# Optimization experiments

Hardware: AMD Instinct MI355X
Metric: run time of the kernel (lower is better)

Reference implementation:

```python
import jax, jax.numpy as jnp
import numpy as np

B, C, F, T = 4, 64, 64, 128
IC = 32  # inter_channels = C // 2
EPS = 1e-5  # BatchNorm eps


def _conv1x1(x, w, b=None):
    # x: (B, Cin, H, W), w: (Cout, Cin)
    y = jnp.einsum('bchw,oc->bohw', x, w)
    if b is not None:
        y = y + b[None, :, None, None]
    return y


def _maxpool2(x):
    b, c, h, w = x.shape
    return x.reshape(b, c, h // 2, 2, w // 2, 2).max(axis=(3, 5))


def _pos_score(fsz, tsz, h2_w):
    # positional encoding is (fpos, tpos) in [0,1]; the 2->1 conv head makes the
    # pos_delta contribution separable: score(n,m) = s(n) - s(m)
    fpos = jnp.linspace(0.0, 1.0, fsz)
    tpos = jnp.linspace(0.0, 1.0, tsz)
    return (h2_w[0] * fpos[:, None] + h2_w[1] * tpos[None, :]).reshape(-1)


def setup_inputs() -> dict:
    key = jax.random.key(0)
    ks = jax.random.split(key, 16)
    s = 0.05
    inp = {
        'x': jax.random.normal(ks[0], (B, C, F, T), dtype=jnp.float32),
        'psi_w': jax.random.normal(ks[1], (IC, C)) * s,
        'psi_b': jax.random.normal(ks[2], (IC,)) * s,
        'theta_w': jax.random.normal(ks[3], (IC, C)) * s,
        'theta_b': jax.random.normal(ks[4], (IC,)) * s,
        'phi_w': jax.random.normal(ks[5], (IC, C)) * s,
        'phi_b': jax.random.normal(ks[6], (IC,)) * s,
        'h0_w': jax.random.normal(ks[7], (IC,)) * s,
        'h1_w': jax.random.normal(ks[8], (IC,)) * s,
        'h2_w': jax.random.normal(ks[9], (2,)) * s,
        'W_w': jax.random.normal(ks[10], (C, IC + 1)) * s,
        'W_b': jax.random.normal(ks[11], (C,)) * s,
        'bn_gamma': jax.random.normal(ks[12], (C,)) * s + 1.0,
        'bn_beta': jax.random.normal(ks[13], (C,)) * s,
        'bn_mean': jax.random.normal(ks[14], (C,)) * s,
        'bn_var': jax.random.uniform(ks[15], (C,), minval=0.5, maxval=1.5),
    }
    return inp


def reference(x, psi_w, psi_b, theta_w, theta_b, phi_w, phi_b,
              h0_w, h1_w, h2_w, W_w, W_b, bn_gamma, bn_beta, bn_mean, bn_var):
    Bs, Cs, Fs, Ts = x.shape
    N = Fs * Ts
    M = (Fs // 2) * (Ts // 2)

    psi_x = _maxpool2(_conv1x1(x, psi_w, psi_b))      # (B, IC, F/2, T/2)
    theta_x = _conv1x1(x, theta_w, theta_b)           # (B, IC, F, T)
    phi_x = _maxpool2(_conv1x1(x, phi_w, phi_b))      # (B, IC, F/2, T/2)

    # additive attention scores: relu(head0(theta) + head1(phi) + head2(pos_delta))
    t_score = jnp.einsum('bcft,c->bft', theta_x, h0_w).reshape(Bs, N)   # (B, N)
    p_score = jnp.einsum('bcft,c->bft', phi_x, h1_w).reshape(Bs, M)     # (B, M)
    a = _pos_score(Fs, Ts, h2_w)             # (N,) query pos contribution
    bpos = _pos_score(Fs // 2, Ts // 2, h2_w)  # (M,) key pos contribution
    f = jax.nn.relu((t_score + a[None, :])[:, :, None]
                    + (p_score - bpos[None, :])[:, None, :])  # (B, N, M)

    f_div = f / jnp.asarray(M, f.dtype)
    psi_flat = psi_x.reshape(Bs, IC, M)
    y = jnp.einsum('bnm,bcm->bcn', f_div, psi_flat).reshape(Bs, IC, Fs, Ts)

    # r_structure_type='zero' -> structure feature is zeros (1 extra channel)
    structure = jnp.zeros((Bs, 1, Fs, Ts), dtype=y.dtype)
    y = jnp.concatenate([y, structure], axis=1)       # (B, IC+1, F, T)

    wy = _conv1x1(y, W_w, W_b)                        # (B, C, F, T)
    inv = bn_gamma / jnp.sqrt(bn_var + EPS)
    wy = wy * inv[None, :, None, None] + (bn_beta - bn_mean * inv)[None, :, None, None]
    return wy + x
```

## Files before the change

kernel.cpp:

```cpp
#include <hip/hip_runtime.h>

#define B_ 4
#define C_ 64
#define F_ 64
#define T_ 128
#define IC_ 32
#define N_ 8192
#define M_ 2048

#define OFF_U      0
#define OFF_PSI2   32768
#define OFF_V      294912
#define OFF_VS     303104
#define OFF_Q0     311296
#define OFF_Q1     835840
#define WS_FLOATS  1360384

__device__ __align__(16) float g_ws[WS_FLOATS];
__device__ int g_perm[B_ * M_];

__global__ __launch_bounds__(256) void k_front(
    const float* __restrict__ x,
    const float* __restrict__ psi_w, const float* __restrict__ psi_b,
    const float* __restrict__ theta_w, const float* __restrict__ theta_b,
    const float* __restrict__ phi_w, const float* __restrict__ phi_b,
    const float* __restrict__ h0_w, const float* __restrict__ h1_w,
    const float* __restrict__ h2_w)
{
    float* __restrict__ ws = g_ws;
    __shared__ __align__(16) float xs[64 * 64];
    __shared__ float pw[32 * 65];
    __shared__ float fw[32 * 65];
    __shared__ float wt_l[64];

    const int tid = threadIdx.x;
    const int bid = blockIdx.x;
    const int b = bid >> 7;
    const int rem = bid & 127;
    const int fh = rem >> 2;
    const int q = rem & 3;
    const int c0 = q * 32;

    for (int idx = tid; idx < 4096; idx += 256) {
        int c = idx >> 6, r2 = (idx >> 5) & 1, tl = idx & 31;
        xs[idx] = x[(((size_t)b * 64 + c) * 64 + (2 * fh + r2)) * 128 + c0 + tl];
    }
    for (int idx = tid; idx < 2048; idx += 256) {
        int o = idx >> 6, c = idx & 63;
        pw[o * 65 + c] = psi_w[idx];
        fw[o * 65 + c] = phi_w[idx];
    }
    if (tid < 64) {
        float acc = 0.f;
        for (int o2 = 0; o2 < 32; ++o2)
            acc += h0_w[o2] * theta_w[o2 * 64 + tid];
        wt_l[tid] = acc;
    }
    __syncthreads();

    const float h20 = h2_w[0], h21 = h2_w[1];

    {
        const int o = tid & 31, g = tid >> 5;
        const float pb = psi_b[o], fb = phi_b[o], h1 = h1_w[o];
        float sp[2][4] = {{0,0,0,0},{0,0,0,0}};
        float sf[2][4] = {{0,0,0,0},{0,0,0,0}};
        const int hc0 = g, hc1 = g + 8;
        for (int c = 0; c < 64; ++c) {
            const float pwv = pw[o * 65 + c];
            const float fwv = fw[o * 65 + c];
            const float2 xa0 = *(const float2*)&xs[c * 64 + 2 * hc0];
            const float2 xb0 = *(const float2*)&xs[c * 64 + 32 + 2 * hc0];
            const float2 xa1 = *(const float2*)&xs[c * 64 + 2 * hc1];
            const float2 xb1 = *(const float2*)&xs[c * 64 + 32 + 2 * hc1];
            sp[0][0] += pwv * xa0.x; sp[0][1] += pwv * xa0.y;
            sp[0][2] += pwv * xb0.x; sp[0][3] += pwv * xb0.y;
            sf[0][0] += fwv * xa0.x; sf[0][1] += fwv * xa0.y;
            sf[0][2] += fwv * xb0.x; sf[0][3] += fwv * xb0.y;
            sp[1][0] += pwv * xa1.x; sp[1][1] += pwv * xa1.y;
            sp[1][2] += pwv * xb1.x; sp[1][3] += pwv * xb1.y;
            sf[1][0] += fwv * xa1.x; sf[1][1] += fwv * xa1.y;
            sf[1][2] += fwv * xb1.x; sf[1][3] += fwv * xb1.y;
        }
#pragma unroll
        for (int h = 0; h < 2; ++h) {
            const int hc = h ? hc1 : hc0;
            const float psiv = fmaxf(fmaxf(sp[h][0], sp[h][1]), fmaxf(sp[h][2], sp[h][3])) + pb;
            const float phiv = fmaxf(fmaxf(sf[h][0], sf[h][1]), fmaxf(sf[h][2], sf[h][3])) + fb;
            const int m = fh * 64 + q * 16 + hc;
            ws[OFF_PSI2 + ((size_t)b * 2048 + m) * 32 + o] = psiv;
            float tv = h1 * phiv;
            for (int mask = 1; mask < 32; mask <<= 1)
                tv += __shfl_xor(tv, mask, 64);
            if (o == 0) {
                const float bpos = h20 * (fh * (1.0f / 31.0f))
                                 + h21 * ((q * 16 + hc) * (1.0f / 63.0f));
                ws[OFF_V + b * 2048 + m] = tv - bpos;
            }
        }
    }

    if (tid < 64) {
        const int r2 = tid >> 5, tl = tid & 31;
        float acc = 0.f;
        for (int c = 0; c < 64; ++c)
            acc += xs[c * 64 + r2 * 32 + tl] * wt_l[c];
        float tb_ = 0.f;
        for (int o2 = 0; o2 < 32; ++o2)
            tb_ += h0_w[o2] * theta_b[o2];
        const int f = 2 * fh + r2, tt = c0 + tl;
        const int n = f * 128 + tt;
        const float a = h20 * (f * (1.0f / 63.0f)) + h21 * (tt * (1.0f / 127.0f));
        ws[OFF_U + b * 8192 + n] = acc + tb_ + a;
    }
}

__global__ __launch_bounds__(256) void k_rank()
{
    float* __restrict__ ws = g_ws;
    __shared__ __align__(16) float vl[2048];
    __shared__ int part[256];
    const int tid = threadIdx.x;
    const int b = blockIdx.x >> 7, chunk = blockIdx.x & 127;
    const float* v = ws + OFF_V + b * 2048;
    for (int i = tid; i < 2048; i += 256) vl[i] = v[i];
    __syncthreads();

    const int ml = tid & 15, jq = tid >> 4;
    const int m = chunk * 16 + ml;
    const float vm = vl[m];
    int cnt = 0;
    const float4* v4 = (const float4*)vl;
    const int j0 = jq * 32;
    for (int j4 = j0; j4 < j0 + 32; ++j4) {
        const float4 vv = v4[j4];
        const int jb = j4 * 4;
        cnt += (vv.x > vm) || (vv.x == vm && (jb    ) < m);
        cnt += (vv.y > vm) || (vv.y == vm && (jb + 1) < m);
        cnt += (vv.z > vm) || (vv.z == vm && (jb + 2) < m);
        cnt += (vv.w > vm) || (vv.w == vm && (jb + 3) < m);
    }
    part[tid] = cnt;
    __syncthreads();
    if (tid < 16) {
        int r = 0;
#pragma unroll
        for (int j = 0; j < 16; ++j) r += part[j * 16 + tid];
        ws[OFF_VS + b * 2048 + r] = vl[chunk * 16 + tid];
        g_perm[b * 2048 + r] = chunk * 16 + tid;
    }
}

__global__ __launch_bounds__(512) void k_scan(
    const float* __restrict__ W_w)
{
    float* __restrict__ ws = g_ws;
    __shared__ float Wrow[32];
    __shared__ float a0[512], a1[512];
    const int tid = threadIdx.x;
    const int b = blockIdx.x >> 6, o = blockIdx.x & 63;
    if (tid < 32) Wrow[tid] = W_w[o * 33 + tid];
    __syncthreads();

    const int* perm = g_perm + b * 2048;
    const float* vs = ws + OFF_VS + b * 2048;
    const float* psi2 = ws + OFF_PSI2 + (size_t)b * 2048 * 32;

    float zl[4], vlv[4];
    float s0 = 0.f, s1 = 0.f;
    const int base = tid * 4;
#pragma unroll
    for (int qq = 0; qq < 4; ++qq) {
        const int i = base + qq;
        const int mp = perm[i];
        const float4* pr = (const float4*)(psi2 + (size_t)mp * 32);
        float z = 0.f;
#pragma unroll
        for (int w = 0; w < 8; ++w) {
            const float4 p4 = pr[w];
            z += Wrow[4 * w] * p4.x + Wrow[4 * w + 1] * p4.y
               + Wrow[4 * w + 2] * p4.z + Wrow[4 * w + 3] * p4.w;
        }
        const float vv = vs[i];
        zl[qq] = z; vlv[qq] = vv;
        s0 += z; s1 += vv * z;
    }
    a0[tid] = s0; a1[tid] = s1;
    __syncthreads();
    for (int off = 1; off < 512; off <<= 1) {
        const float t0_ = (tid >= off) ? a0[tid - off] : 0.f;
        const float t1_ = (tid >= off) ? a1[tid - off] : 0.f;
        __syncthreads();
        a0[tid] += t0_; a1[tid] += t1_;
        __syncthreads();
    }
    float r0 = a0[tid] - s0, r1 = a1[tid] - s1;
    float* Q0 = ws + OFF_Q0 + (size_t)b * 2049 * 64;
    float* Q1 = ws + OFF_Q1 + (size_t)b * 2049 * 64;
#pragma unroll
    for (int qq = 0; qq < 4; ++qq) {
        r0 += zl[qq]; r1 += vlv[qq] * zl[qq];
        Q0[(size_t)(base + qq + 1) * 64 + o] = r0;
        Q1[(size_t)(base + qq + 1) * 64 + o] = r1;
    }
    if (tid == 0) { Q0[o] = 0.f; Q1[o] = 0.f; }
}

__global__ __launch_bounds__(512) void k_out(
    const float* __restrict__ x,
    const float* __restrict__ W_b,
    const float* __restrict__ bn_g, const float* __restrict__ bn_b,
    const float* __restrict__ bn_m, const float* __restrict__ bn_v,
    float* __restrict__ out)
{
    const float* __restrict__ ws = g_ws;
    __shared__ float tileb[64 * 65];
    __shared__ int karr[64];
    __shared__ float uarr[64];

    const int tid = threadIdx.x;
    const int b = blockIdx.x >> 7, tile = blockIdx.x & 127;
    const int n0 = tile * 64;

    const float* vs = ws + OFF_VS + b * 2048;
    if (tid < 64) {
        const float u = ws[OFF_U + b * 8192 + n0 + tid];
        const float thr = -u;
        int lo = 0, hi = 2048;
        while (lo < hi) {
            const int mid = (lo + hi) >> 1;
            if (vs[mid] > thr) lo = mid + 1; else hi = mid;
        }
        karr[tid] = lo;
        uarr[tid] = u;
    }
    __syncthreads();

    const int lane = tid & 63, w = tid >> 6;
    const float inv = bn_g[lane] * __frsqrt_rn(bn_v[lane] + 1e-5f);
    const float sft = W_b[lane] * inv + bn_b[lane] - bn_m[lane] * inv;
    const float* Q0 = ws + OFF_Q0 + (size_t)b * 2049 * 64;
    const float* Q1 = ws + OFF_Q1 + (size_t)b * 2049 * 64;

    for (int nl = w; nl < 64; nl += 8) {
        const int k = karr[nl];
        const float u = uarr[nl];
        const float q0 = Q0[(size_t)k * 64 + lane];
        const float q1 = Q1[(size_t)k * 64 + lane];
        const float raw = (u * q0 + q1) * (1.0f / 2048.0f);
        tileb[lane * 65 + nl] = raw * inv + sft;
    }
    __syncthreads();

    for (int idx = tid; idx < 2048; idx += 512) {
        const int o = idx >> 5, j2 = idx & 31;
        const size_t gi = ((size_t)b * 64 + o) * 8192 + n0 + 2 * j2;
        const float2 xv = *(const float2*)&x[gi];
        float2 r;
        r.x = tileb[o * 65 + 2 * j2] + xv.x;
        r.y = tileb[o * 65 + 2 * j2 + 1] + xv.y;
        *(float2*)&out[gi] = r;
    }
}

extern "C" void kernel_launch(void* const* d_in, const int* in_sizes, int n_in,
                              void* d_out, int out_size, void* d_ws, size_t ws_size,
                              hipStream_t stream)
{
    (void)in_sizes; (void)n_in; (void)out_size; (void)d_ws; (void)ws_size;
    const float* x       = (const float*)d_in[0];
    const float* psi_w   = (const float*)d_in[1];
    const float* psi_b   = (const float*)d_in[2];
    const float* theta_w = (const float*)d_in[3];
    const float* theta_b = (const float*)d_in[4];
    const float* phi_w   = (const float*)d_in[5];
    const float* phi_b   = (const float*)d_in[6];
    const float* h0_w    = (const float*)d_in[7];
    const float* h1_w    = (const float*)d_in[8];
    const float* h2_w    = (const float*)d_in[9];
    const float* W_w     = (const float*)d_in[10];
    const float* W_b     = (const float*)d_in[11];
    const float* bn_g    = (const float*)d_in[12];
    const float* bn_b    = (const float*)d_in[13];
    const float* bn_m    = (const float*)d_in[14];
    const float* bn_v    = (const float*)d_in[15];
    float* out = (float*)d_out;

    k_front<<<dim3(512), dim3(256), 0, stream>>>(x, psi_w, psi_b, theta_w, theta_b,
                                                 phi_w, phi_b, h0_w, h1_w, h2_w);
    k_rank<<<dim3(512), dim3(256), 0, stream>>>();
    k_scan<<<dim3(256), dim3(512), 0, stream>>>(W_w);
    k_out<<<dim3(512), dim3(512), 0, stream>>>(x, W_b, bn_g, bn_b, bn_m, bn_v, out);
}
```

Baseline: 137.4 us.

## Fuse four phases into one cooperative kernel with grid-wide syncs

Merges the front, rank, scan and output kernels into a single cooperative launch of 512 blocks of 256 threads, using grid.sync between phases. The goal is to remove the launch gaps between the four kernels, and it falls back to separate launches if the cooperative launch fails. It also switches the x tile load to float4 and regroups the front accumulation around float4 shared reads. Every phase now uses 256 threads, so the scan does 8 elements per thread and the output loops stride by 4. Grid syncs carry their own barrier cost, and the shared buffer sized for the largest phase may limit occupancy.

```diff
diff --git a/kernel.cpp b/kernel.cpp
--- a/kernel.cpp
+++ b/kernel.cpp
@@ -1,4 +1,7 @@
 #include <hip/hip_runtime.h>
+#include <hip/hip_cooperative_groups.h>
+
+namespace cg = cooperative_groups;
 
 #define B_ 4
 #define C_ 64
@@ -19,7 +22,7 @@
 __device__ __align__(16) float g_ws[WS_FLOATS];
 __device__ int g_perm[B_ * M_];
 
-__global__ __launch_bounds__(256) void k_front(
+__device__ __forceinline__ void phase_front(float* smem,
     const float* __restrict__ x,
     const float* __restrict__ psi_w, const float* __restrict__ psi_b,
     const float* __restrict__ theta_w, const float* __restrict__ theta_b,
@@ -28,10 +31,10 @@
     const float* __restrict__ h2_w)
 {
     float* __restrict__ ws = g_ws;
-    __shared__ __align__(16) float xs[64 * 64];
-    __shared__ float pw[32 * 65];
-    __shared__ float fw[32 * 65];
-    __shared__ float wt_l[64];
+    float* xs   = smem;
+    float* pw   = smem + 4096;
+    float* fw   = smem + 6176;
+    float* wt_l = smem + 8256;
 
     const int tid = threadIdx.x;
     const int bid = blockIdx.x;
@@ -41,12 +44,13 @@
     const int q = rem & 3;
     const int c0 = q * 32;
 
-    for (int idx = tid; idx < 4096; idx += 256) {
-        int c = idx >> 6, r2 = (idx >> 5) & 1, tl = idx & 31;
-        xs[idx] = x[(((size_t)b * 64 + c) * 64 + (2 * fh + r2)) * 128 + c0 + tl];
+    for (int idx = tid; idx < 1024; idx += 256) {
+        const int c = idx >> 4, r2 = (idx >> 3) & 1, t4 = idx & 7;
+        const float4 v = *(const float4*)&x[(((size_t)b * 64 + c) * 64 + (2 * fh + r2)) * 128 + c0 + 4 * t4];
+        *(float4*)&xs[c * 64 + r2 * 32 + 4 * t4] = v;
     }
     for (int idx = tid; idx < 2048; idx += 256) {
-        int o = idx >> 6, c = idx & 63;
+        const int o = idx >> 6, c = idx & 63;
         pw[o * 65 + c] = psi_w[idx];
         fw[o * 65 + c] = phi_w[idx];
     }
@@ -65,26 +69,23 @@
         const float pb = psi_b[o], fb = phi_b[o], h1 = h1_w[o];
         float sp[2][4] = {{0,0,0,0},{0,0,0,0}};
         float sf[2][4] = {{0,0,0,0},{0,0,0,0}};
-        const int hc0 = g, hc1 = g + 8;
         for (int c = 0; c < 64; ++c) {
             const float pwv = pw[o * 65 + c];
             const float fwv = fw[o * 65 + c];
-            const float2 xa0 = *(const float2*)&xs[c * 64 + 2 * hc0];
-            const float2 xb0 = *(const float2*)&xs[c * 64 + 32 + 2 * hc0];
-            const float2 xa1 = *(const float2*)&xs[c * 64 + 2 * hc1];
-            const float2 xb1 = *(const float2*)&xs[c * 64 + 32 + 2 * hc1];
-            sp[0][0] += pwv * xa0.x; sp[0][1] += pwv * xa0.y;
-            sp[0][2] += pwv * xb0.x; sp[0][3] += pwv * xb0.y;
-            sf[0][0] += fwv * xa0.x; sf[0][1] += fwv * xa0.y;
-            sf[0][2] += fwv * xb0.x; sf[0][3] += fwv * xb0.y;
-            sp[1][0] += pwv * xa1.x; sp[1][1] += pwv * xa1.y;
-            sp[1][2] += pwv * xb1.x; sp[1][3] += pwv * xb1.y;
-            sf[1][0] += fwv * xa1.x; sf[1][1] += fwv * xa1.y;
-            sf[1][2] += fwv * xb1.x; sf[1][3] += fwv * xb1.y;
+            const float4 r0v = *(const float4*)&xs[c * 64 + 4 * g];
+            const float4 r1v = *(const float4*)&xs[c * 64 + 32 + 4 * g];
+            sp[0][0] += pwv * r0v.x; sp[0][1] += pwv * r0v.y;
+            sp[0][2] += pwv * r1v.x; sp[0][3] += pwv * r1v.y;
+            sp[1][0] += pwv * r0v.z; sp[1][1] += pwv * r0v.w;
+            sp[1][2] += pwv * r1v.z; sp[1][3] += pwv * r1v.w;
+            sf[0][0] += fwv * r0v.x; sf[0][1] += fwv * r0v.y;
+            sf[0][2] += fwv * r1v.x; sf[0][3] += fwv * r1v.y;
+            sf[1][0] += fwv * r0v.z; sf[1][1] += fwv * r0v.w;
+            sf[1][2] += fwv * r1v.z; sf[1][3] += fwv * r1v.w;
         }
 #pragma unroll
         for (int h = 0; h < 2; ++h) {
-            const int hc = h ? hc1 : hc0;
+            const int hc = 2 * g + h;
             const float psiv = fmaxf(fmaxf(sp[h][0], sp[h][1]), fmaxf(sp[h][2], sp[h][3])) + pb;
             const float phiv = fmaxf(fmaxf(sf[h][0], sf[h][1]), fmaxf(sf[h][2], sf[h][3])) + fb;
             const int m = fh * 64 + q * 16 + hc;
@@ -115,11 +116,11 @@
     }
 }
 
-__global__ __launch_bounds__(256) void k_rank()
+__device__ __forceinline__ void phase_rank(float* smem)
 {
     float* __restrict__ ws = g_ws;
-    __shared__ __align__(16) float vl[2048];
-    __shared__ int part[256];
+    float* vl = smem;
+    int* part = (int*)(smem + 2048);
     const int tid = threadIdx.x;
     const int b = blockIdx.x >> 7, chunk = blockIdx.x & 127;
     const float* v = ws + OFF_V + b * 2048;
@@ -151,12 +152,13 @@
     }
 }
 
-__global__ __launch_bounds__(512) void k_scan(
-    const float* __restrict__ W_w)
-{
+__device__ __forceinline__ void phase_scan(float* smem, const float* __restrict__ W_w)
+{
+    if (blockIdx.x >= 256) return;
     float* __restrict__ ws = g_ws;
-    __shared__ float Wrow[32];
-    __shared__ float a0[512], a1[512];
+    float* a0 = smem;
+    float* a1 = smem + 256;
+    float* Wrow = smem + 512;
     const int tid = threadIdx.x;
     const int b = blockIdx.x >> 6, o = blockIdx.x & 63;
     if (tid < 32) Wrow[tid] = W_w[o * 33 + tid];
@@ -166,11 +168,11 @@
     const float* vs = ws + OFF_VS + b * 2048;
     const float* psi2 = ws + OFF_PSI2 + (size_t)b * 2048 * 32;
 
-    float zl[4], vlv[4];
+    float zl[8], vlv[8];
     float s0 = 0.f, s1 = 0.f;
-    const int base = tid * 4;
-#pragma unroll
-    for (int qq = 0; qq < 4; ++qq) {
+    const int base = tid * 8;
+#pragma unroll
+    for (int qq = 0; qq < 8; ++qq) {
         const int i = base + qq;
         const int mp = perm[i];
         const float4* pr = (const float4*)(psi2 + (size_t)mp * 32);
@@ -187,7 +189,7 @@
     }
     a0[tid] = s0; a1[tid] = s1;
     __syncthreads();
-    for (int off = 1; off < 512; off <<= 1) {
+    for (int off = 1; off < 256; off <<= 1) {
         const float t0_ = (tid >= off) ? a0[tid - off] : 0.f;
         const float t1_ = (tid >= off) ? a1[tid - off] : 0.f;
         __syncthreads();
@@ -198,7 +200,7 @@
     float* Q0 = ws + OFF_Q0 + (size_t)b * 2049 * 64;
     float* Q1 = ws + OFF_Q1 + (size_t)b * 2049 * 64;
 #pragma unroll
-    for (int qq = 0; qq < 4; ++qq) {
+    for (int qq = 0; qq < 8; ++qq) {
         r0 += zl[qq]; r1 += vlv[qq] * zl[qq];
         Q0[(size_t)(base + qq + 1) * 64 + o] = r0;
         Q1[(size_t)(base + qq + 1) * 64 + o] = r1;
@@ -206,7 +208,7 @@
     if (tid == 0) { Q0[o] = 0.f; Q1[o] = 0.f; }
 }
 
-__global__ __launch_bounds__(512) void k_out(
+__device__ __forceinline__ void phase_out(float* smem,
     const float* __restrict__ x,
     const float* __restrict__ W_b,
     const float* __restrict__ bn_g, const float* __restrict__ bn_b,
@@ -214,9 +216,9 @@
     float* __restrict__ out)
 {
     const float* __restrict__ ws = g_ws;
-    __shared__ float tileb[64 * 65];
-    __shared__ int karr[64];
-    __shared__ float uarr[64];
+    float* tileb = smem;
+    int* karr = (int*)(smem + 4160);
+    float* uarr = smem + 4224;
 
     const int tid = threadIdx.x;
     const int b = blockIdx.x >> 7, tile = blockIdx.x & 127;
@@ -242,7 +244,7 @@
     const float* Q0 = ws + OFF_Q0 + (size_t)b * 2049 * 64;
     const float* Q1 = ws + OFF_Q1 + (size_t)b * 2049 * 64;
 
-    for (int nl = w; nl < 64; nl += 8) {
+    for (int nl = w; nl < 64; nl += 4) {
         const int k = karr[nl];
         const float u = uarr[nl];
         const float q0 = Q0[(size_t)k * 64 + lane];
@@ -252,7 +254,7 @@
     }
     __syncthreads();
 
-    for (int idx = tid; idx < 2048; idx += 512) {
+    for (int idx = tid; idx < 2048; idx += 256) {
         const int o = idx >> 5, j2 = idx & 31;
         const size_t gi = ((size_t)b * 64 + o) * 8192 + n0 + 2 * j2;
         const float2 xv = *(const float2*)&x[gi];
@@ -261,6 +263,56 @@
         r.y = tileb[o * 65 + 2 * j2 + 1] + xv.y;
         *(float2*)&out[gi] = r;
     }
+}
+
+__global__ __launch_bounds__(256, 2) void k_fused(
+    const float* x,
+    const float* psi_w, const float* psi_b,
+    const float* theta_w, const float* theta_b,
+    const float* phi_w, const float* phi_b,
+    const float* h0_w, const float* h1_w, const float* h2_w,
+    const float* W_w, const float* W_b,
+    const float* bn_g, const float* bn_b, const float* bn_m, const float* bn_v,
+    float* out)
+{
+    __shared__ __align__(16) float smem[8384];
+    cg::grid_group grid = cg::this_grid();
+
+    phase_front(smem, x, psi_w, psi_b, theta_w, theta_b, phi_w, phi_b, h0_w, h1_w, h2_w);
+    __threadfence(); grid.sync();
+    phase_rank(smem);
+    __threadfence(); grid.sync();
+    phase_scan(smem, W_w);
+    __threadfence(); grid.sync();
+    phase_out(smem, x, W_b, bn_g, bn_b, bn_m, bn_v, out);
+}
+
+__global__ __launch_bounds__(256) void k1(
+    const float* x, const float* psi_w, const float* psi_b,
+    const float* theta_w, const float* theta_b,
+    const float* phi_w, const float* phi_b,
+    const float* h0_w, const float* h1_w, const float* h2_w)
+{
+    __shared__ __align__(16) float smem[8384];
+    phase_front(smem, x, psi_w, psi_b, theta_w, theta_b, phi_w, phi_b, h0_w, h1_w, h2_w);
+}
+__global__ __launch_bounds__(256) void k2()
+{
+    __shared__ __align__(16) float smem[2304];
+    phase_rank(smem);
+}
+__global__ __launch_bounds__(256) void k3(const float* W_w)
+{
+    __shared__ __align__(16) float smem[544];
+    phase_scan(smem, W_w);
+}
+__global__ __launch_bounds__(256) void k4(
+    const float* x, const float* W_b,
+    const float* bn_g, const float* bn_b, const float* bn_m, const float* bn_v,
+    float* out)
+{
+    __shared__ __align__(16) float smem[4288];
+    phase_out(smem, x, W_b, bn_g, bn_b, bn_m, bn_v, out);
 }
 
 extern "C" void kernel_launch(void* const* d_in, const int* in_sizes, int n_in,
@@ -286,9 +338,20 @@
     const float* bn_v    = (const float*)d_in[15];
     float* out = (float*)d_out;
 
-    k_front<<<dim3(512), dim3(256), 0, stream>>>(x, psi_w, psi_b, theta_w, theta_b,
-                                                 phi_w, phi_b, h0_w, h1_w, h2_w);
-    k_rank<<<dim3(512), dim3(256), 0, stream>>>();
-    k_scan<<<dim3(256), dim3(512), 0, stream>>>(W_w);
-    k_out<<<dim3(512), dim3(512), 0, stream>>>(x, W_b, bn_g, bn_b, bn_m, bn_v, out);
-}
+    void* args[] = {
+        (void*)&x, (void*)&psi_w, (void*)&psi_b, (void*)&theta_w, (void*)&theta_b,
+        (void*)&phi_w, (void*)&phi_b, (void*)&h0_w, (void*)&h1_w, (void*)&h2_w,
+        (void*)&W_w, (void*)&W_b, (void*)&bn_g, (void*)&bn_b, (void*)&bn_m,
+        (void*)&bn_v, (void*)&out
+    };
+    hipError_t e = hipLaunchCooperativeKernel((const void*)k_fused,
+                                              dim3(512), dim3(256), args, 0, stream);
+    if (e != hipSuccess) {
+        (void)hipGetLastError();
+        k1<<<dim3(512), dim3(256), 0, stream>>>(x, psi_w, psi_b, theta_w, theta_b,
+                                                phi_w, phi_b, h0_w, h1_w, h2_w);
+        k2<<<dim3(512), dim3(256), 0, stream>>>();
+        k3<<<dim3(256), dim3(256), 0, stream>>>(W_w);
+        k4<<<dim3(512), dim3(256), 0, stream>>>(x, W_b, bn_g, bn_b, bn_m, bn_v, out);
+    }
+}
```

Result: slower. 453.9 us (+230.2%).
